# Kernel tuning notes

Measured on AMD Instinct MI355X. Metric: run time of the kernel, lower is better.

The kernel has to match this reference:

```python
import jax, jax.numpy as jnp
import numpy as np
from jax import lax


def ternarize(w):
    # TWN-style ternarization: threshold delta = 0.7*mean|w|, scale alpha =
    # mean |w| over surviving entries; straight-through in backward.
    aw = jnp.abs(w)
    delta = 0.7 * jnp.mean(aw)
    mask = (aw > delta).astype(w.dtype)
    alpha = jnp.sum(aw * mask) / jnp.maximum(jnp.sum(mask), 1.0)
    q = alpha * jnp.sign(w) * mask
    return w + lax.stop_gradient(q - w)


def conv2d(x, w, b):
    # x: [N,C,H,W], w: [O,I,kh,kw]
    y = lax.conv_general_dilated(x, w, window_strides=(1, 1), padding='VALID',
                                 dimension_numbers=('NCHW', 'OIHW', 'NCHW'))
    return y + b[None, :, None, None]


def maxpool2(x):
    return lax.reduce_window(x, -jnp.inf, lax.max,
                             window_dimensions=(1, 1, 2, 2),
                             window_strides=(1, 1, 2, 2), padding='VALID')


def setup_inputs() -> dict:
    key = jax.random.key(0)
    ks = jax.random.split(key, 11)
    n_classes = 10
    x = jax.random.normal(ks[0], (1024, 1, 32, 32), dtype=jnp.float32)
    # Kaiming-ish scaled params
    w1 = jax.random.normal(ks[1], (32, 1, 5, 5), jnp.float32) * (1.0 / np.sqrt(1 * 25))
    b1 = jnp.zeros((32,), jnp.float32)
    w2 = jax.random.normal(ks[2], (64, 32, 5, 5), jnp.float32) * (1.0 / np.sqrt(32 * 25))
    b2 = jnp.zeros((64,), jnp.float32)
    w3 = jax.random.normal(ks[3], (120, 64, 5, 5), jnp.float32) * (1.0 / np.sqrt(64 * 25))
    b3 = jnp.zeros((120,), jnp.float32)
    fw1 = jax.random.normal(ks[4], (84, 120), jnp.float32) * (1.0 / np.sqrt(120))
    fb1 = jnp.zeros((84,), jnp.float32)
    fw2 = jax.random.normal(ks[5], (n_classes, 84), jnp.float32) * (1.0 / np.sqrt(84))
    fb2 = jnp.zeros((n_classes,), jnp.float32)
    return {"x": x, "w1": w1, "b1": b1, "w2": w2, "b2": b2,
            "w3": w3, "b3": b3, "fw1": fw1, "fb1": fb1, "fw2": fw2, "fb2": fb2}


def reference(x, w1, b1, w2, b2, w3, b3, fw1, fb1, fw2, fb2):
    h = jnp.tanh(conv2d(x, ternarize(w1), b1))   # [N,32,28,28]
    h = maxpool2(h)                              # [N,32,14,14]
    h = jnp.tanh(conv2d(h, ternarize(w2), b2))   # [N,64,10,10]
    h = maxpool2(h)                              # [N,64,5,5]
    h = jnp.tanh(conv2d(h, ternarize(w3), b3))   # [N,120,1,1]
    h = h.reshape(h.shape[0], -1)                # [N,120]
    h = jnp.tanh(h @ ternarize(fw1).T + fb1)     # [N,84]
    logits = h @ ternarize(fw2).T + fb2          # [N,n_classes]
    probs = jax.nn.softmax(logits, axis=1)
    return (logits, probs)
```

## Files before the change

kernel.cpp:

```cpp
#include <hip/hip_runtime.h>
#include <hip/hip_bf16.h>
#include <math.h>


typedef __attribute__((ext_vector_type(8))) short bf16x8;
typedef __attribute__((ext_vector_type(4))) float f32x4;

static const size_t OFF_PB    = 0;
static const size_t OFF_W1B   = 256;
static const size_t OFF_W2B   = 1056;
static const size_t OFF_W3B   = 26656;
static const size_t OFF_FW1T  = 129056;
static const size_t OFF_FW2T  = 139136;
static const size_t OFF_P2B   = 139976;
static const size_t OFF_H3    = 959176;

#define BPT 16

__device__ __forceinline__ ushort f2bf(float v) {
    unsigned u = __float_as_uint(v);
    unsigned r = (u + 0x7FFFu + ((u >> 16) & 1u)) >> 16;
    return (ushort)r;
}
__device__ __forceinline__ float bf2f(ushort h) {
    return __uint_as_float((unsigned)h << 16);
}

__device__ __forceinline__ float tanh_fast(float x) {
    float e = __expf(-2.0f * fabsf(x));
    float r = 1.0f - 2.0f * e / (1.0f + e);
    return copysignf(r, x);
}

__device__ __forceinline__ void tensor_select(int tensor,
        const float* w1, const float* w2, const float* w3,
        const float* fw1, const float* fw2,
        const float*& src, int& O, int& K) {
    switch (tensor) {
        case 0: src = w1;  O = 32;  K = 25;   break;
        case 1: src = w2;  O = 64;  K = 800;  break;
        case 2: src = w3;  O = 120; K = 1600; break;
        case 3: src = fw1; O = 84;  K = 120;  break;
        default: src = fw2; O = 10; K = 84;   break;
    }
}

__device__ __forceinline__ float block_sum_256(float v, float* sbuf) {
    #pragma unroll
    for (int off = 32; off > 0; off >>= 1) v += __shfl_down(v, off);
    const int wid = threadIdx.x >> 6;
    if ((threadIdx.x & 63) == 0) sbuf[wid] = v;
    __syncthreads();
    return sbuf[0] + sbuf[1] + sbuf[2] + sbuf[3];
}

__device__ __forceinline__ float alpha_of(const float* pb, int tensor) {
    float s1 = 0.f, c = 0.f;
    #pragma unroll
    for (int i = 0; i < BPT; ++i) {
        s1 += pb[80 + tensor * BPT + i];
        c  += pb[160 + tensor * BPT + i];
    }
    return s1 / fmaxf(c, 1.0f);
}

__global__ __launch_bounds__(256)
void tern_pass1(const float* w1, const float* w2, const float* w3,
                const float* fw1, const float* fw2, float* pb) {
    __shared__ float sbuf[4];
    const int tensor = blockIdx.x / BPT;
    const int blk    = blockIdx.x % BPT;
    const float* src; int O, K;
    tensor_select(tensor, w1, w2, w3, fw1, fw2, src, O, K);
    const int n = O * K;
    float s = 0.f;
    for (int i = blk * 256 + threadIdx.x; i < n; i += BPT * 256)
        s += fabsf(src[i]);
    s = block_sum_256(s, sbuf);
    if (threadIdx.x == 0) pb[tensor * BPT + blk] = s;
}

__global__ __launch_bounds__(256)
void tern_pass2(const float* w1, const float* w2, const float* w3,
                const float* fw1, const float* fw2,
                ushort* w1b, ushort* w2b, ushort* w3b,
                float* fw1t, float* fw2t, float* pb) {
    __shared__ float sbuf[4];
    const int tensor = blockIdx.x / BPT;
    const int blk    = blockIdx.x % BPT;
    const float* src; int O, K;
    tensor_select(tensor, w1, w2, w3, fw1, fw2, src, O, K);
    const int n = O * K;
    float tot = 0.f;
    #pragma unroll
    for (int i = 0; i < BPT; ++i) tot += pb[tensor * BPT + i];
    const float delta = 0.7f * tot / (float)n;

    const ushort BP = 0x3F80u, BN = 0xBF80u;
    float s1 = 0.f, cnt = 0.f;

    if (tensor == 0) {
        for (int j = blk * 256 + threadIdx.x; j < 1024; j += BPT * 256) {
            const int oc = j >> 5, kk = j & 31;
            ushort qb = 0;
            if (kk < 25) {
                float w = src[oc * 25 + kk];
                float aw = fabsf(w);
                if (aw > delta) { s1 += aw; cnt += 1.f; qb = (w > 0.f) ? BP : BN; }
            }
            w1b[j] = qb;
        }
    } else if (tensor == 2) {
        for (int i = blk * 256 + threadIdx.x; i < 128 * 1600; i += BPT * 256) {
            ushort qb = 0;
            if (i < n) {
                float w = src[i];
                float aw = fabsf(w);
                if (aw > delta) { s1 += aw; cnt += 1.f; qb = (w > 0.f) ? BP : BN; }
            }
            w3b[i] = qb;
        }
    } else if (tensor == 1) {
        for (int i = blk * 256 + threadIdx.x; i < n; i += BPT * 256) {
            float w = src[i];
            float aw = fabsf(w);
            ushort qb = 0;
            if (aw > delta) { s1 += aw; cnt += 1.f; qb = (w > 0.f) ? BP : BN; }
            int oc = i / 800;
            int r  = i - oc * 800;
            int ic = r / 25;
            int tap = r - ic * 25;
            w2b[oc * 800 + tap * 32 + ic] = qb;
        }
    } else {
        float* dst = (tensor == 3) ? fw1t : fw2t;
        for (int i = blk * 256 + threadIdx.x; i < n; i += BPT * 256) {
            float w = src[i];
            float aw = fabsf(w);
            float q = 0.f;
            if (aw > delta) { s1 += aw; cnt += 1.f; q = (w > 0.f) ? 1.f : -1.f; }
            int o = i / K;
            int k = i - o * K;
            dst[k * O + o] = q;
        }
    }
    s1 = block_sum_256(s1, sbuf);
    __syncthreads();
    cnt = block_sum_256(cnt, sbuf);
    if (threadIdx.x == 0) {
        pb[80 + tensor * BPT + blk]  = s1;
        pb[160 + tensor * BPT + blk] = cnt;
    }
}

template<int TBASE, int TCNT>
__device__ __forceinline__ void conv2_phase(
        const ushort* __restrict__ w2b, const ushort* sxt,
        int n0, int mt0, int lane, f32x4 acc[4][2]) {
    const int col = lane & 15, quad = lane >> 4;
    bf16x8 bfr[TCNT][2];
    #pragma unroll
    for (int i = 0; i < TCNT; ++i) {
        const int tap = TBASE + i;
        #pragma unroll
        for (int np = 0; np < 2; ++np) {
            const int oc = n0 + np * 16 + col;
            bfr[i][np] = *(const bf16x8*)(w2b + (oc * 25 + tap) * 32 + quad * 8);
        }
    }
    #pragma unroll
    for (int mi = 0; mi < 4; ++mi) {
        int m = (mt0 + mi) * 16 + col;
        m = m < 100 ? m : 99;
        const int oh = m / 10, ow = m - oh * 10;
        const ushort* abase = sxt + (oh * 14 + ow) * 40 + quad * 8;
        #pragma unroll
        for (int i = 0; i < TCNT; ++i) {
            const int tap = TBASE + i;
            const int kh = tap / 5, kw = tap - kh * 5;
            bf16x8 af = *(const bf16x8*)(abase + (kh * 14 + kw) * 40);
            acc[mi][0] = __builtin_amdgcn_mfma_f32_16x16x32_bf16(af, bfr[i][0], acc[mi][0], 0, 0, 0);
            acc[mi][1] = __builtin_amdgcn_mfma_f32_16x16x32_bf16(af, bfr[i][1], acc[mi][1], 0, 0, 0);
        }
    }
}

__global__ __launch_bounds__(256)
void conv12_kernel(const float* __restrict__ x, const ushort* __restrict__ w1b,
                   const float* __restrict__ b1, const ushort* __restrict__ w2b,
                   const float* __restrict__ b2, const float* __restrict__ pb,
                   ushort* __restrict__ p2b) {
    __shared__ __align__(16) char smem[53008];
    ushort* sxb    = (ushort*)smem;
    ushort* A      = (ushort*)(smem + 2048);
    ushort* sxt    = (ushort*)(smem + 2048);
    ushort* hb1    = (ushort*)(smem + 27648);
    float*  hb2    = (float*) (smem + 27648);
    float*  sbias  = (float*) (smem + 52864);
    float*  salpha = (float*) (smem + 52992);

    const int n = blockIdx.x;
    const int t = threadIdx.x;
    const int wave = t >> 6, lane = t & 63;
    const int col = lane & 15, quad = lane >> 4;

    bf16x8 B0 = *(const bf16x8*)(w1b + col * 32 + quad * 8);
    bf16x8 B1 = *(const bf16x8*)(w1b + (col + 16) * 32 + quad * 8);

    {
        float4 v = ((const float4*)(x + (size_t)n * 1024))[t];
        ushort4 q;
        q.x = f2bf(v.x); q.y = f2bf(v.y); q.z = f2bf(v.z); q.w = f2bf(v.w);
        *(ushort4*)(sxb + t * 4) = q;
        if (t < 32) sbias[t] = b1[t];
        if (t == 32) salpha[0] = alpha_of(pb, 0);
        if (t == 33) salpha[1] = alpha_of(pb, 1);
    }
    __syncthreads();

    for (int half = 0; half < 2; ++half) {
        const int base   = half ? 400 : 0;
        const int rows   = half ? 384 : 400;
        const int ntiles = half ? 24  : 25;

        for (int p = base + t; p < base + rows; p += 256) {
            const int pl = p - base;
            const int oh = p / 28, ow = p % 28;
            ushort v[25];
            #pragma unroll
            for (int kh = 0; kh < 5; ++kh) {
                const ushort* r = sxb + (oh + kh) * 32 + ow;
                v[kh * 5 + 0] = r[0]; v[kh * 5 + 1] = r[1]; v[kh * 5 + 2] = r[2];
                v[kh * 5 + 3] = r[3]; v[kh * 5 + 4] = r[4];
            }
            unsigned d[16];
            #pragma unroll
            for (int j = 0; j < 12; ++j)
                d[j] = (unsigned)v[2 * j] | ((unsigned)v[2 * j + 1] << 16);
            d[12] = (unsigned)v[24];
            d[13] = 0u; d[14] = 0u; d[15] = 0u;
            uint4* arow = (uint4*)(A + pl * 32);
            uint4 w0; w0.x = d[0];  w0.y = d[1];  w0.z = d[2];  w0.w = d[3];
            uint4 w1; w1.x = d[4];  w1.y = d[5];  w1.z = d[6];  w1.w = d[7];
            uint4 w2; w2.x = d[8];  w2.y = d[9];  w2.z = d[10]; w2.w = d[11];
            uint4 w3; w3.x = d[12]; w3.y = d[13]; w3.z = d[14]; w3.w = d[15];
            arow[0] = w0; arow[1] = w1; arow[2] = w2; arow[3] = w3;
        }
        __syncthreads();

        for (int tile = wave; tile < ntiles; tile += 4) {
            bf16x8 af = *(const bf16x8*)(A + (tile * 16 + col) * 32 + quad * 8);
            f32x4 z = {};
            f32x4 c0 = __builtin_amdgcn_mfma_f32_16x16x32_bf16(af, B0, z, 0, 0, 0);
            f32x4 c1 = __builtin_amdgcn_mfma_f32_16x16x32_bf16(af, B1, z, 0, 0, 0);
            const int p = base + tile * 16 + quad * 4;
            const int oh = p / 28, ow2 = (p % 28) >> 1;
            ushort2 h0, h1;
            h0.x = f2bf(fmaxf(c0[0], c0[1])); h0.y = f2bf(fmaxf(c0[2], c0[3]));
            h1.x = f2bf(fmaxf(c1[0], c1[1])); h1.y = f2bf(fmaxf(c1[2], c1[3]));
            *(ushort2*)(hb1 + col * 394 + oh * 14 + ow2) = h0;
            *(ushort2*)(hb1 + (col + 16) * 394 + oh * 14 + ow2) = h1;
        }
        __syncthreads();
    }

    {
        const float a1 = salpha[0];
        for (int idx = t; idx < 6272; idx += 256) {
            const int oc = idx & 31, pos = idx >> 5;
            const int ph = pos / 14, pw = pos - ph * 14;
            const ushort* hp = hb1 + oc * 394 + (2 * ph) * 14 + pw;
            float m = fmaxf(bf2f(hp[0]), bf2f(hp[14]));
            sxt[pos * 40 + oc] = f2bf(tanh_fast(fmaf(a1, m, sbias[oc])));
        }
    }
    __syncthreads();

    const int n0  = (wave & 1) * 32;
    const int mt0 = (wave >> 1) * 4;
    f32x4 acc2[4][2] = {};
    conv2_phase<0, 13>(w2b, sxt, n0, mt0, lane, acc2);
    conv2_phase<13, 12>(w2b, sxt, n0, mt0, lane, acc2);

    {
        #pragma unroll
        for (int mi = 0; mi < 4; ++mi) {
            const int mrow = (mt0 + mi) * 16 + quad * 4;
            if (mrow < 100) {
                #pragma unroll
                for (int np = 0; np < 2; ++np) {
                    const int oc = n0 + np * 16 + col;
                    float2 hm;
                    hm.x = fmaxf(acc2[mi][np][0], acc2[mi][np][1]);
                    hm.y = fmaxf(acc2[mi][np][2], acc2[mi][np][3]);
                    *(float2*)(&hb2[oc * 50 + (mrow >> 1)]) = hm;
                }
            }
        }
    }
    __syncthreads();

    const float a2 = salpha[1];
    for (int idx = t; idx < 1600; idx += 256) {
        const int oc = idx / 25, r = idx - oc * 25;
        const int ph = r / 5, pw = r - ph * 5;
        const float* hb = &hb2[oc * 50 + ph * 10 + pw];
        float m = fmaxf(hb[0], hb[5]);
        p2b[(size_t)n * 1600 + idx] = f2bf(tanh_fast(fmaf(a2, m, b2[oc])));
    }
}

template<int STEPS>
__device__ __forceinline__ void conv3_chunk(const ushort* Abase, const ushort* B0,
                                            const ushort* B1, f32x4& acc0, f32x4& acc1) {
    #pragma unroll
    for (int s = 0; s < STEPS; ++s) {
        bf16x8 af = *(const bf16x8*)(Abase + s * 32);
        bf16x8 b0 = *(const bf16x8*)(B0 + s * 32);
        bf16x8 b1 = *(const bf16x8*)(B1 + s * 32);
        acc0 = __builtin_amdgcn_mfma_f32_16x16x32_bf16(af, b0, acc0, 0, 0, 0);
        acc1 = __builtin_amdgcn_mfma_f32_16x16x32_bf16(af, b1, acc1, 0, 0, 0);
    }
}

__global__ __launch_bounds__(256)
void conv3_mfma(const ushort* __restrict__ p2b, const ushort* __restrict__ w3b,
                const float* __restrict__ b3, const float* __restrict__ pb,
                float* __restrict__ h3) {
    __shared__ float red[4][64][8];
    __shared__ float salpha;
    const int t = threadIdx.x;
    const int wave = t >> 6, lane = t & 63;
    const int mt = blockIdx.x >> 2;
    const int npair = blockIdx.x & 3;
    const int col = lane & 15, quad = lane >> 4;
    const int kstart = (wave < 2) ? wave * 13 : 26 + (wave - 2) * 12;

    if (t == 0) salpha = alpha_of(pb, 2);

    const ushort* Abase = p2b + (size_t)(mt * 16 + col) * 1600 + kstart * 32 + quad * 8;
    const ushort* B0 = w3b + (size_t)(npair * 32 + col) * 1600 + kstart * 32 + quad * 8;
    const ushort* B1 = B0 + 16 * 1600;

    f32x4 acc0 = {}, acc1 = {};
    if (wave < 2) conv3_chunk<13>(Abase, B0, B1, acc0, acc1);
    else          conv3_chunk<12>(Abase, B0, B1, acc0, acc1);

    #pragma unroll
    for (int r = 0; r < 4; ++r) {
        red[wave][lane][r]     = acc0[r];
        red[wave][lane][4 + r] = acc1[r];
    }
    __syncthreads();

    {
        const float a3 = salpha;
        const int l = t & 63, vh = t >> 6;
        const int lcol = l & 15, lquad = l >> 4;
        const int img = mt * 16 + lquad * 4 + vh;
        #pragma unroll
        for (int j = 0; j < 2; ++j) {
            const int v = j * 4 + vh;
            float s = red[0][l][v] + red[1][l][v] + red[2][l][v] + red[3][l][v];
            const int oc = npair * 32 + j * 16 + lcol;
            if (oc < 120) h3[(size_t)img * 120 + oc] = tanh_fast(fmaf(a3, s, b3[oc]));
        }
    }
}

__global__ __launch_bounds__(128)
void fc_kernel(const float* __restrict__ h3, const float* __restrict__ fw1t,
               const float* __restrict__ fb1, const float* __restrict__ fw2t,
               const float* __restrict__ fb2, const float* __restrict__ pb,
               float* __restrict__ out) {
    const int n = blockIdx.x;
    __shared__ float sh[120];
    __shared__ float sh4[84];
    __shared__ float sl[10];
    __shared__ float salpha[2];
    const int t = threadIdx.x;
    if (t < 120) sh[t] = h3[(size_t)n * 120 + t];
    if (t == 120) salpha[0] = alpha_of(pb, 3);
    if (t == 121) salpha[1] = alpha_of(pb, 4);
    __syncthreads();
    if (t < 84) {
        const float af1 = salpha[0];
        float a = 0.f;
        #pragma unroll 4
        for (int k = 0; k < 120; ++k) a = fmaf(fw1t[k * 84 + t], sh[k], a);
        sh4[t] = tanh_fast(fmaf(af1, a, fb1[t]));
    }
    __syncthreads();
    if (t < 10) {
        const float af2 = salpha[1];
        float a = 0.f;
        #pragma unroll 4
        for (int k = 0; k < 84; ++k) a = fmaf(fw2t[k * 10 + t], sh4[k], a);
        const float lg = fmaf(af2, a, fb2[t]);
        sl[t] = lg;
        out[(size_t)n * 10 + t] = lg;
    }
    __syncthreads();
    if (t < 10) {
        float m = -INFINITY;
        #pragma unroll
        for (int i = 0; i < 10; ++i) m = fmaxf(m, sl[i]);
        float s = 0.f;
        #pragma unroll
        for (int i = 0; i < 10; ++i) s += expf(sl[i] - m);
        out[10240 + (size_t)n * 10 + t] = expf(sl[t] - m) / s;
    }
}

extern "C" void kernel_launch(void* const* d_in, const int* in_sizes, int n_in,
                              void* d_out, int out_size, void* d_ws, size_t ws_size,
                              hipStream_t stream) {
    const float* x   = (const float*)d_in[0];
    const float* w1  = (const float*)d_in[1];
    const float* b1  = (const float*)d_in[2];
    const float* w2  = (const float*)d_in[3];
    const float* b2  = (const float*)d_in[4];
    const float* w3  = (const float*)d_in[5];
    const float* b3  = (const float*)d_in[6];
    const float* fw1 = (const float*)d_in[7];
    const float* fb1 = (const float*)d_in[8];
    const float* fw2 = (const float*)d_in[9];
    const float* fb2 = (const float*)d_in[10];

    float* ws = (float*)d_ws;
    float*  pb   = ws + OFF_PB;
    ushort* w1b  = (ushort*)(ws + OFF_W1B);
    ushort* w2b  = (ushort*)(ws + OFF_W2B);
    ushort* w3b  = (ushort*)(ws + OFF_W3B);
    float*  fw1t = ws + OFF_FW1T;
    float*  fw2t = ws + OFF_FW2T;
    ushort* p2b  = (ushort*)(ws + OFF_P2B);
    float*  h3   = ws + OFF_H3;
    float*  out  = (float*)d_out;

    tern_pass1<<<5 * BPT, 256, 0, stream>>>(w1, w2, w3, fw1, fw2, pb);
    tern_pass2<<<5 * BPT, 256, 0, stream>>>(w1, w2, w3, fw1, fw2,
                                            w1b, w2b, w3b, fw1t, fw2t, pb);
    conv12_kernel<<<1024, 256, 0, stream>>>(x, w1b, b1, w2b, b2, pb, p2b);
    conv3_mfma<<<256, 256, 0, stream>>>(p2b, w3b, b3, pb, h3);
    fc_kernel<<<1024, 128, 0, stream>>>(h3, fw1t, fb1, fw2t, fb2, pb, out);
}
```

Before: 163.5 us.

## Gather conv1 im2col operands directly into registers and shrink LDS footprint

Drops the explicit im2col staging of conv1 patches in shared memory. Each lane now gathers its eight tap values for the MFMA A operand straight from the bf16 input tile, using precomputed tap offsets and a validity mask. That removes the two-half loop and its extra barriers. The shared-memory layout is compacted so the conv2 input overlays the freed region, and its row stride is narrowed from 40 to 36 elements, which lowers LDS per block and may allow more resident blocks. The risk is that the 72-byte stride breaks 16-byte alignment for the vector LDS loads in conv2, which could split them or add bank conflicts.

Result: slower. 183.6 us (+12.3%).

```diff
diff --git a/kernel.cpp b/kernel.cpp
--- a/kernel.cpp
+++ b/kernel.cpp
@@ -5,6 +5,8 @@
 
 typedef __attribute__((ext_vector_type(8))) short bf16x8;
 typedef __attribute__((ext_vector_type(4))) float f32x4;
+
+#define SXT_STRIDE 36
 
 static const size_t OFF_PB    = 0;
 static const size_t OFF_W1B   = 256;
@@ -173,12 +175,12 @@
         int m = (mt0 + mi) * 16 + col;
         m = m < 100 ? m : 99;
         const int oh = m / 10, ow = m - oh * 10;
-        const ushort* abase = sxt + (oh * 14 + ow) * 40 + quad * 8;
+        const ushort* abase = sxt + (oh * 14 + ow) * SXT_STRIDE + quad * 8;
         #pragma unroll
         for (int i = 0; i < TCNT; ++i) {
             const int tap = TBASE + i;
             const int kh = tap / 5, kw = tap - kh * 5;
-            bf16x8 af = *(const bf16x8*)(abase + (kh * 14 + kw) * 40);
+            bf16x8 af = *(const bf16x8*)(abase + (kh * 14 + kw) * SXT_STRIDE);
             acc[mi][0] = __builtin_amdgcn_mfma_f32_16x16x32_bf16(af, bfr[i][0], acc[mi][0], 0, 0, 0);
             acc[mi][1] = __builtin_amdgcn_mfma_f32_16x16x32_bf16(af, bfr[i][1], acc[mi][1], 0, 0, 0);
         }
@@ -190,14 +192,13 @@
                    const float* __restrict__ b1, const ushort* __restrict__ w2b,
                    const float* __restrict__ b2, const float* __restrict__ pb,
                    ushort* __restrict__ p2b) {
-    __shared__ __align__(16) char smem[53008];
+    __shared__ __align__(16) char smem[39464];
     ushort* sxb    = (ushort*)smem;
-    ushort* A      = (ushort*)(smem + 2048);
-    ushort* sxt    = (ushort*)(smem + 2048);
-    ushort* hb1    = (ushort*)(smem + 27648);
-    float*  hb2    = (float*) (smem + 27648);
-    float*  sbias  = (float*) (smem + 52864);
-    float*  salpha = (float*) (smem + 52992);
+    ushort* sxt    = (ushort*)smem;
+    ushort* hb1    = (ushort*)(smem + 14112);
+    float*  hb2    = (float*) (smem + 14112);
+    float*  sbias  = (float*) (smem + 39328);
+    float*  salpha = (float*) (smem + 39456);
 
     const int n = blockIdx.x;
     const int t = threadIdx.x;
@@ -206,6 +207,19 @@
 
     bf16x8 B0 = *(const bf16x8*)(w1b + col * 32 + quad * 8);
     bf16x8 B1 = *(const bf16x8*)(w1b + (col + 16) * 32 + quad * 8);
+
+    int  dj[8];
+    bool vj[8];
+    {
+        const int t0 = quad * 8;
+        #pragma unroll
+        for (int j = 0; j < 8; ++j) {
+            const int tap = t0 + j;
+            const int kh = tap / 5, kw = tap - kh * 5;
+            vj[j] = (tap < 25);
+            dj[j] = vj[j] ? (kh * 32 + kw) : 0;
+        }
+    }
 
     {
         float4 v = ((const float4*)(x + (size_t)n * 1024))[t];
@@ -218,51 +232,28 @@
     }
     __syncthreads();
 
-    for (int half = 0; half < 2; ++half) {
-        const int base   = half ? 400 : 0;
-        const int rows   = half ? 384 : 400;
-        const int ntiles = half ? 24  : 25;
-
-        for (int p = base + t; p < base + rows; p += 256) {
-            const int pl = p - base;
-            const int oh = p / 28, ow = p % 28;
-            ushort v[25];
-            #pragma unroll
-            for (int kh = 0; kh < 5; ++kh) {
-                const ushort* r = sxb + (oh + kh) * 32 + ow;
-                v[kh * 5 + 0] = r[0]; v[kh * 5 + 1] = r[1]; v[kh * 5 + 2] = r[2];
-                v[kh * 5 + 3] = r[3]; v[kh * 5 + 4] = r[4];
-            }
-            unsigned d[16];
-            #pragma unroll
-            for (int j = 0; j < 12; ++j)
-                d[j] = (unsigned)v[2 * j] | ((unsigned)v[2 * j + 1] << 16);
-            d[12] = (unsigned)v[24];
-            d[13] = 0u; d[14] = 0u; d[15] = 0u;
-            uint4* arow = (uint4*)(A + pl * 32);
-            uint4 w0; w0.x = d[0];  w0.y = d[1];  w0.z = d[2];  w0.w = d[3];
-            uint4 w1; w1.x = d[4];  w1.y = d[5];  w1.z = d[6];  w1.w = d[7];
-            uint4 w2; w2.x = d[8];  w2.y = d[9];  w2.z = d[10]; w2.w = d[11];
-            uint4 w3; w3.x = d[12]; w3.y = d[13]; w3.z = d[14]; w3.w = d[15];
-            arow[0] = w0; arow[1] = w1; arow[2] = w2; arow[3] = w3;
-        }
-        __syncthreads();
-
-        for (int tile = wave; tile < ntiles; tile += 4) {
-            bf16x8 af = *(const bf16x8*)(A + (tile * 16 + col) * 32 + quad * 8);
-            f32x4 z = {};
-            f32x4 c0 = __builtin_amdgcn_mfma_f32_16x16x32_bf16(af, B0, z, 0, 0, 0);
-            f32x4 c1 = __builtin_amdgcn_mfma_f32_16x16x32_bf16(af, B1, z, 0, 0, 0);
-            const int p = base + tile * 16 + quad * 4;
-            const int oh = p / 28, ow2 = (p % 28) >> 1;
-            ushort2 h0, h1;
-            h0.x = f2bf(fmaxf(c0[0], c0[1])); h0.y = f2bf(fmaxf(c0[2], c0[3]));
-            h1.x = f2bf(fmaxf(c1[0], c1[1])); h1.y = f2bf(fmaxf(c1[2], c1[3]));
-            *(ushort2*)(hb1 + col * 394 + oh * 14 + ow2) = h0;
-            *(ushort2*)(hb1 + (col + 16) * 394 + oh * 14 + ow2) = h1;
-        }
-        __syncthreads();
-    }
+    for (int tile = wave; tile < 49; tile += 4) {
+        const int m = tile * 16 + col;
+        const int oh = m / 28, ow = m - oh * 28;
+        const int base = oh * 32 + ow;
+        bf16x8 af;
+        #pragma unroll
+        for (int j = 0; j < 8; ++j) {
+            ushort r = sxb[base + dj[j]];
+            af[j] = (short)(vj[j] ? r : (ushort)0);
+        }
+        f32x4 z = {};
+        f32x4 c0 = __builtin_amdgcn_mfma_f32_16x16x32_bf16(af, B0, z, 0, 0, 0);
+        f32x4 c1 = __builtin_amdgcn_mfma_f32_16x16x32_bf16(af, B1, z, 0, 0, 0);
+        const int p = tile * 16 + quad * 4;
+        const int poh = p / 28, pow2 = (p % 28) >> 1;
+        ushort2 h0, h1;
+        h0.x = f2bf(fmaxf(c0[0], c0[1])); h0.y = f2bf(fmaxf(c0[2], c0[3]));
+        h1.x = f2bf(fmaxf(c1[0], c1[1])); h1.y = f2bf(fmaxf(c1[2], c1[3]));
+        *(ushort2*)(hb1 + col * 394 + poh * 14 + pow2) = h0;
+        *(ushort2*)(hb1 + (col + 16) * 394 + poh * 14 + pow2) = h1;
+    }
+    __syncthreads();
 
     {
         const float a1 = salpha[0];
@@ -271,7 +262,7 @@
             const int ph = pos / 14, pw = pos - ph * 14;
             const ushort* hp = hb1 + oc * 394 + (2 * ph) * 14 + pw;
             float m = fmaxf(bf2f(hp[0]), bf2f(hp[14]));
-            sxt[pos * 40 + oc] = f2bf(tanh_fast(fmaf(a1, m, sbias[oc])));
+            sxt[pos * SXT_STRIDE + oc] = f2bf(tanh_fast(fmaf(a1, m, sbias[oc])));
         }
     }
     __syncthreads();
```

## Fuse conv3 with FC layers and softmax into one kernel per 4 images

Applied to the files above, without the earlier changes.

Replaces the separate conv3 MFMA kernel and per-image FC kernel with one fused kernel that handles 4 images per block. Each wave now covers 32 output channels over the full K=1600 reduction, so the cross-wave LDS reduction goes away. The h3 intermediate stays in shared memory and one launch is removed. The cost is that only 4 of the 16 MFMA rows carry useful images, which wastes matrix throughput and re-reads the w3 weights in every block.

After: 179.8 us. +9.9%, slower.

```diff
diff --git a/kernel.cpp b/kernel.cpp
--- a/kernel.cpp
+++ b/kernel.cpp
@@ -13,7 +13,6 @@
 static const size_t OFF_FW1T  = 129056;
 static const size_t OFF_FW2T  = 139136;
 static const size_t OFF_P2B   = 139976;
-static const size_t OFF_H3    = 959176;
 
 #define BPT 16
 
@@ -310,105 +309,84 @@
     }
 }
 
-template<int STEPS>
-__device__ __forceinline__ void conv3_chunk(const ushort* Abase, const ushort* B0,
-                                            const ushort* B1, f32x4& acc0, f32x4& acc1) {
-    #pragma unroll
-    for (int s = 0; s < STEPS; ++s) {
+__global__ __launch_bounds__(256)
+void conv3fc_kernel(const ushort* __restrict__ p2b, const ushort* __restrict__ w3b,
+                    const float* __restrict__ b3, const float* __restrict__ fw1t,
+                    const float* __restrict__ fb1, const float* __restrict__ fw2t,
+                    const float* __restrict__ fb2, const float* __restrict__ pb,
+                    float* __restrict__ out) {
+    __shared__ float sh3[4][120];
+    __shared__ float sh4[4][84];
+    __shared__ float slog[4][10];
+    __shared__ float salpha[3];
+    const int t = threadIdx.x;
+    const int wave = t >> 6, lane = t & 63;
+    const int col = lane & 15, quad = lane >> 4;
+    const int i0 = blockIdx.x * 4;
+
+    if (t < 3) salpha[t] = alpha_of(pb, t + 2);
+
+    const int img = i0 + (col < 4 ? col : 3);
+    const ushort* Abase = p2b + (size_t)img * 1600 + quad * 8;
+    const ushort* B0 = w3b + (size_t)(wave * 32 + col) * 1600 + quad * 8;
+    const ushort* B1 = B0 + 16 * 1600;
+
+    f32x4 acc0 = {}, acc1 = {};
+    #pragma unroll 5
+    for (int s = 0; s < 50; ++s) {
         bf16x8 af = *(const bf16x8*)(Abase + s * 32);
         bf16x8 b0 = *(const bf16x8*)(B0 + s * 32);
         bf16x8 b1 = *(const bf16x8*)(B1 + s * 32);
         acc0 = __builtin_amdgcn_mfma_f32_16x16x32_bf16(af, b0, acc0, 0, 0, 0);
         acc1 = __builtin_amdgcn_mfma_f32_16x16x32_bf16(af, b1, acc1, 0, 0, 0);
     }
-}
-
-__global__ __launch_bounds__(256)
-void conv3_mfma(const ushort* __restrict__ p2b, const ushort* __restrict__ w3b,
-                const float* __restrict__ b3, const float* __restrict__ pb,
-                float* __restrict__ h3) {
-    __shared__ float red[4][64][8];
-    __shared__ float salpha;
-    const int t = threadIdx.x;
-    const int wave = t >> 6, lane = t & 63;
-    const int mt = blockIdx.x >> 2;
-    const int npair = blockIdx.x & 3;
-    const int col = lane & 15, quad = lane >> 4;
-    const int kstart = (wave < 2) ? wave * 13 : 26 + (wave - 2) * 12;
-
-    if (t == 0) salpha = alpha_of(pb, 2);
-
-    const ushort* Abase = p2b + (size_t)(mt * 16 + col) * 1600 + kstart * 32 + quad * 8;
-    const ushort* B0 = w3b + (size_t)(npair * 32 + col) * 1600 + kstart * 32 + quad * 8;
-    const ushort* B1 = B0 + 16 * 1600;
-
-    f32x4 acc0 = {}, acc1 = {};
-    if (wave < 2) conv3_chunk<13>(Abase, B0, B1, acc0, acc1);
-    else          conv3_chunk<12>(Abase, B0, B1, acc0, acc1);
-
-    #pragma unroll
-    for (int r = 0; r < 4; ++r) {
-        red[wave][lane][r]     = acc0[r];
-        red[wave][lane][4 + r] = acc1[r];
+    __syncthreads();
+
+    if (quad == 0) {
+        const float a3 = salpha[0];
+        #pragma unroll
+        for (int r = 0; r < 4; ++r) {
+            const int oc0 = wave * 32 + col;
+            sh3[r][oc0] = tanh_fast(fmaf(a3, acc0[r], b3[oc0]));
+            const int oc1 = oc0 + 16;
+            if (oc1 < 120) sh3[r][oc1] = tanh_fast(fmaf(a3, acc1[r], b3[oc1]));
+        }
     }
     __syncthreads();
 
     {
-        const float a3 = salpha;
-        const int l = t & 63, vh = t >> 6;
-        const int lcol = l & 15, lquad = l >> 4;
-        const int img = mt * 16 + lquad * 4 + vh;
-        #pragma unroll
-        for (int j = 0; j < 2; ++j) {
-            const int v = j * 4 + vh;
-            float s = red[0][l][v] + red[1][l][v] + red[2][l][v] + red[3][l][v];
-            const int oc = npair * 32 + j * 16 + lcol;
-            if (oc < 120) h3[(size_t)img * 120 + oc] = tanh_fast(fmaf(a3, s, b3[oc]));
-        }
-    }
-}
-
-__global__ __launch_bounds__(128)
-void fc_kernel(const float* __restrict__ h3, const float* __restrict__ fw1t,
-               const float* __restrict__ fb1, const float* __restrict__ fw2t,
-               const float* __restrict__ fb2, const float* __restrict__ pb,
-               float* __restrict__ out) {
-    const int n = blockIdx.x;
-    __shared__ float sh[120];
-    __shared__ float sh4[84];
-    __shared__ float sl[10];
-    __shared__ float salpha[2];
-    const int t = threadIdx.x;
-    if (t < 120) sh[t] = h3[(size_t)n * 120 + t];
-    if (t == 120) salpha[0] = alpha_of(pb, 3);
-    if (t == 121) salpha[1] = alpha_of(pb, 4);
-    __syncthreads();
-    if (t < 84) {
-        const float af1 = salpha[0];
-        float a = 0.f;
+        const float af1 = salpha[1];
+        for (int idx = t; idx < 336; idx += 256) {
+            const int im = idx / 84, oc = idx - im * 84;
+            float s = 0.f;
+            #pragma unroll 4
+            for (int k = 0; k < 120; ++k) s = fmaf(fw1t[k * 84 + oc], sh3[im][k], s);
+            sh4[im][oc] = tanh_fast(fmaf(af1, s, fb1[oc]));
+        }
+    }
+    __syncthreads();
+
+    if (t < 40) {
+        const float af2 = salpha[2];
+        const int im = t / 10, oc = t - im * 10;
+        float s = 0.f;
         #pragma unroll 4
-        for (int k = 0; k < 120; ++k) a = fmaf(fw1t[k * 84 + t], sh[k], a);
-        sh4[t] = tanh_fast(fmaf(af1, a, fb1[t]));
-    }
-    __syncthreads();
-    if (t < 10) {
-        const float af2 = salpha[1];
-        float a = 0.f;
-        #pragma unroll 4
-        for (int k = 0; k < 84; ++k) a = fmaf(fw2t[k * 10 + t], sh4[k], a);
-        const float lg = fmaf(af2, a, fb2[t]);
-        sl[t] = lg;
-        out[(size_t)n * 10 + t] = lg;
-    }
-    __syncthreads();
-    if (t < 10) {
+        for (int k = 0; k < 84; ++k) s = fmaf(fw2t[k * 10 + oc], sh4[im][k], s);
+        const float lg = fmaf(af2, s, fb2[oc]);
+        slog[im][oc] = lg;
+        out[(size_t)(i0 + im) * 10 + oc] = lg;
+    }
+    __syncthreads();
+
+    if (t < 40) {
+        const int im = t / 10, oc = t - im * 10;
         float m = -INFINITY;
         #pragma unroll
-        for (int i = 0; i < 10; ++i) m = fmaxf(m, sl[i]);
-        float s = 0.f;
-        #pragma unroll
-        for (int i = 0; i < 10; ++i) s += expf(sl[i] - m);
-        out[10240 + (size_t)n * 10 + t] = expf(sl[t] - m) / s;
+        for (int i = 0; i < 10; ++i) m = fmaxf(m, slog[im][i]);
+        float ssum = 0.f;
+        #pragma unroll
+        for (int i = 0; i < 10; ++i) ssum += expf(slog[im][i] - m);
+        out[10240 + (size_t)(i0 + im) * 10 + oc] = expf(slog[im][oc] - m) / ssum;
     }
 }
 
@@ -435,13 +413,12 @@
     float*  fw1t = ws + OFF_FW1T;
     float*  fw2t = ws + OFF_FW2T;
     ushort* p2b  = (ushort*)(ws + OFF_P2B);
-    float*  h3   = ws + OFF_H3;
     float*  out  = (float*)d_out;
 
     tern_pass1<<<5 * BPT, 256, 0, stream>>>(w1, w2, w3, fw1, fw2, pb);
     tern_pass2<<<5 * BPT, 256, 0, stream>>>(w1, w2, w3, fw1, fw2,
                                             w1b, w2b, w3b, fw1t, fw2t, pb);
     conv12_kernel<<<1024, 256, 0, stream>>>(x, w1b, b1, w2b, b2, pb, p2b);
-    conv3_mfma<<<256, 256, 0, stream>>>(p2b, w3b, b3, pb, h3);
-    fc_kernel<<<1024, 128, 0, stream>>>(h3, fw1t, fb1, fw2t, fb2, pb, out);
-}
+    conv3fc_kernel<<<256, 256, 0, stream>>>(p2b, w3b, b3, fw1t, fb1,
+                                            fw2t, fb2, pb, out);
+}
```

## Shrink conv1 LDS footprint with 4-chunk im2col and channel-interleaved pool buffer

Applied to the files above, without the earlier changes.

Splits conv1's im2col staging into four smaller chunks instead of two halves, pads A rows to 36 elements, and stores the horizontally pooled conv1 outputs position-major with channels interleaved. Bias moves into a register. Together these cut shared memory from about 53KB to about 41KB, which may allow more blocks per CU and reduce LDS bank conflicts on the pool and transpose stage. In exchange it adds two extra barrier rounds, split 8-byte A loads, and scalar 2-byte stores to hb1.

New measurement: 161.7 us (median of 2 runs). Within noise of the previous version (-1.1%).

```diff
diff --git a/kernel.cpp b/kernel.cpp
--- a/kernel.cpp
+++ b/kernel.cpp
@@ -190,14 +190,13 @@
                    const float* __restrict__ b1, const ushort* __restrict__ w2b,
                    const float* __restrict__ b2, const float* __restrict__ pb,
                    ushort* __restrict__ p2b) {
-    __shared__ __align__(16) char smem[53008];
-    ushort* sxb    = (ushort*)smem;
-    ushort* A      = (ushort*)(smem + 2048);
-    ushort* sxt    = (ushort*)(smem + 2048);
-    ushort* hb1    = (ushort*)(smem + 27648);
-    float*  hb2    = (float*) (smem + 27648);
-    float*  sbias  = (float*) (smem + 52864);
-    float*  salpha = (float*) (smem + 52992);
+    __shared__ __align__(16) char smem[40776];
+    ushort* A      = (ushort*)smem;
+    ushort* sxt    = (ushort*)smem;
+    ushort* hb1    = (ushort*)(smem + 15680);
+    float*  hb2    = (float*) (smem + 15680);
+    ushort* sxb    = (ushort*)(smem + 38720);
+    float*  salpha = (float*) (smem + 40768);
 
     const int n = blockIdx.x;
     const int t = threadIdx.x;
@@ -206,72 +205,81 @@
 
     bf16x8 B0 = *(const bf16x8*)(w1b + col * 32 + quad * 8);
     bf16x8 B1 = *(const bf16x8*)(w1b + (col + 16) * 32 + quad * 8);
+    const float b1reg = b1[t & 31];
 
     {
         float4 v = ((const float4*)(x + (size_t)n * 1024))[t];
         ushort4 q;
         q.x = f2bf(v.x); q.y = f2bf(v.y); q.z = f2bf(v.z); q.w = f2bf(v.w);
         *(ushort4*)(sxb + t * 4) = q;
-        if (t < 32) sbias[t] = b1[t];
-        if (t == 32) salpha[0] = alpha_of(pb, 0);
-        if (t == 33) salpha[1] = alpha_of(pb, 1);
-    }
-    __syncthreads();
-
-    for (int half = 0; half < 2; ++half) {
-        const int base   = half ? 400 : 0;
-        const int rows   = half ? 384 : 400;
-        const int ntiles = half ? 24  : 25;
-
-        for (int p = base + t; p < base + rows; p += 256) {
-            const int pl = p - base;
+        if (t == 0) salpha[0] = alpha_of(pb, 0);
+        if (t == 1) salpha[1] = alpha_of(pb, 1);
+    }
+    __syncthreads();
+
+    #pragma unroll
+    for (int c = 0; c < 4; ++c) {
+        const int tbase = c * 13;
+        const int ct    = (c == 3) ? 10 : 13;
+        const int pbase = tbase * 16;
+        const int rows  = ct * 16;
+
+        for (int r = t; r < rows; r += 256) {
+            const int p = pbase + r;
             const int oh = p / 28, ow = p % 28;
             ushort v[25];
             #pragma unroll
             for (int kh = 0; kh < 5; ++kh) {
-                const ushort* r = sxb + (oh + kh) * 32 + ow;
-                v[kh * 5 + 0] = r[0]; v[kh * 5 + 1] = r[1]; v[kh * 5 + 2] = r[2];
-                v[kh * 5 + 3] = r[3]; v[kh * 5 + 4] = r[4];
+                const ushort* rr = sxb + (oh + kh) * 32 + ow;
+                v[kh*5+0]=rr[0]; v[kh*5+1]=rr[1]; v[kh*5+2]=rr[2];
+                v[kh*5+3]=rr[3]; v[kh*5+4]=rr[4];
             }
-            unsigned d[16];
+            uint2* arow = (uint2*)(A + r * 36);
             #pragma unroll
-            for (int j = 0; j < 12; ++j)
-                d[j] = (unsigned)v[2 * j] | ((unsigned)v[2 * j + 1] << 16);
-            d[12] = (unsigned)v[24];
-            d[13] = 0u; d[14] = 0u; d[15] = 0u;
-            uint4* arow = (uint4*)(A + pl * 32);
-            uint4 w0; w0.x = d[0];  w0.y = d[1];  w0.z = d[2];  w0.w = d[3];
-            uint4 w1; w1.x = d[4];  w1.y = d[5];  w1.z = d[6];  w1.w = d[7];
-            uint4 w2; w2.x = d[8];  w2.y = d[9];  w2.z = d[10]; w2.w = d[11];
-            uint4 w3; w3.x = d[12]; w3.y = d[13]; w3.z = d[14]; w3.w = d[15];
-            arow[0] = w0; arow[1] = w1; arow[2] = w2; arow[3] = w3;
+            for (int j = 0; j < 6; ++j) {
+                uint2 w;
+                w.x = (unsigned)v[4*j]   | ((unsigned)v[4*j+1] << 16);
+                w.y = (unsigned)v[4*j+2] | ((unsigned)v[4*j+3] << 16);
+                arow[j] = w;
+            }
+            uint2 w6; w6.x = (unsigned)v[24]; w6.y = 0u;
+            arow[6] = w6;
+            uint2 w7; w7.x = 0u; w7.y = 0u;
+            arow[7] = w7;
         }
         __syncthreads();
 
-        for (int tile = wave; tile < ntiles; tile += 4) {
-            bf16x8 af = *(const bf16x8*)(A + (tile * 16 + col) * 32 + quad * 8);
+        for (int tl = wave; tl < ct; tl += 4) {
+            const ushort* ap = A + (tl * 16 + col) * 36 + quad * 8;
+            ushort4 lo = *(const ushort4*)ap;
+            ushort4 hi = *(const ushort4*)(ap + 4);
+            bf16x8 af;
+            af[0]=(short)lo.x; af[1]=(short)lo.y; af[2]=(short)lo.z; af[3]=(short)lo.w;
+            af[4]=(short)hi.x; af[5]=(short)hi.y; af[6]=(short)hi.z; af[7]=(short)hi.w;
             f32x4 z = {};
             f32x4 c0 = __builtin_amdgcn_mfma_f32_16x16x32_bf16(af, B0, z, 0, 0, 0);
             f32x4 c1 = __builtin_amdgcn_mfma_f32_16x16x32_bf16(af, B1, z, 0, 0, 0);
-            const int p = base + tile * 16 + quad * 4;
+            const int p = pbase + tl * 16 + quad * 4;
             const int oh = p / 28, ow2 = (p % 28) >> 1;
-            ushort2 h0, h1;
-            h0.x = f2bf(fmaxf(c0[0], c0[1])); h0.y = f2bf(fmaxf(c0[2], c0[3]));
-            h1.x = f2bf(fmaxf(c1[0], c1[1])); h1.y = f2bf(fmaxf(c1[2], c1[3]));
-            *(ushort2*)(hb1 + col * 394 + oh * 14 + ow2) = h0;
-            *(ushort2*)(hb1 + (col + 16) * 394 + oh * 14 + ow2) = h1;
+            const int pos = oh * 14 + ow2;
+            hb1[pos * 32 + col]            = f2bf(fmaxf(c0[0], c0[1]));
+            hb1[(pos + 1) * 32 + col]      = f2bf(fmaxf(c0[2], c0[3]));
+            hb1[pos * 32 + col + 16]       = f2bf(fmaxf(c1[0], c1[1]));
+            hb1[(pos + 1) * 32 + col + 16] = f2bf(fmaxf(c1[2], c1[3]));
         }
         __syncthreads();
     }
 
     {
         const float a1 = salpha[0];
+        const int oc = t & 31;
         for (int idx = t; idx < 6272; idx += 256) {
-            const int oc = idx & 31, pos = idx >> 5;
-            const int ph = pos / 14, pw = pos - ph * 14;
-            const ushort* hp = hb1 + oc * 394 + (2 * ph) * 14 + pw;
-            float m = fmaxf(bf2f(hp[0]), bf2f(hp[14]));
-            sxt[pos * 40 + oc] = f2bf(tanh_fast(fmaf(a1, m, sbias[oc])));
+            const int pos2 = idx >> 5;
+            const int ph = pos2 / 14, pw = pos2 - ph * 14;
+            const int in0 = (2 * ph) * 14 + pw;
+            float m = fmaxf(bf2f(hb1[in0 * 32 + oc]),
+                            bf2f(hb1[(in0 + 14) * 32 + oc]));
+            sxt[pos2 * 40 + oc] = f2bf(tanh_fast(fmaf(a1, m, b1reg)));
         }
     }
     __syncthreads();
```
